# Kernel optimization log

Hardware: AMD Instinct MI355X
Metric: run time of the kernel (lower is better)

Reference implementation:

```python
import jax, jax.numpy as jnp
import numpy as np

N = 8192

def _gcn_layer(x, src, dst, W, b, norm_out, norm_in, activation=None):
    # DGL GraphConv, norm='both': D_in^{-1/2} A D_out^{-1/2} X W + b
    xw = x @ W                              # [N, out] (weight first: in>=out)
    m = (xw * norm_out[:, None])[src]       # gather per-edge messages [E, out]
    agg = jax.ops.segment_sum(m, dst, num_segments=N)
    h = agg * norm_in[:, None] + b
    return activation(h) if activation is not None else h


def setup_inputs() -> dict:
    key = jax.random.key(0)
    k1, k2, k3, k4, k5 = jax.random.split(key, 5)
    E = 262144
    in_dim, h1, h2 = 512, 256, 64
    features = jax.random.normal(k1, (N, in_dim), dtype=jnp.float32)
    src = jax.random.randint(k2, (E,), 0, N)
    dst = jax.random.randint(k3, (E,), 0, N)
    W1 = jax.random.normal(k4, (in_dim, h1), dtype=jnp.float32) / np.sqrt(in_dim)
    b1 = jnp.zeros((h1,), dtype=jnp.float32)
    W2 = jax.random.normal(k5, (h1, h2), dtype=jnp.float32) / np.sqrt(h1)
    b2 = jnp.zeros((h2,), dtype=jnp.float32)
    return {"features": features, "src": src, "dst": dst,
            "W1": W1, "b1": b1, "W2": W2, "b2": b2}


def reference(features, src, dst, W1, b1, W2, b2):
    # Degrees and symmetric normalization (clamp(min=1) as in DGL GraphConv).
    ones = jnp.ones(src.shape[0], dtype=features.dtype)
    deg_out = jax.ops.segment_sum(ones, src, num_segments=N)
    deg_in = jax.ops.segment_sum(ones, dst, num_segments=N)
    norm_out = jnp.maximum(deg_out, 1.0) ** -0.5
    norm_in = jnp.maximum(deg_in, 1.0) ** -0.5
    # Encoder (dropout is identity in eval mode).
    h = _gcn_layer(features, src, dst, W1, b1, norm_out, norm_in, jax.nn.relu)
    z = _gcn_layer(h, src, dst, W2, b2, norm_out, norm_in, None)
    # Dot-product decoder.
    adj_rec = jax.nn.sigmoid(z @ z.T)       # [N, N]
    return adj_rec
```

## Files before the change

### kernel.cpp

```cpp
#include <hip/hip_runtime.h>
#include <hip/hip_bf16.h>
#include <math.h>

#define NNODES 8192
#define NEDGES 262144
#define INDIM  512
#define H1     256
#define H2     64

typedef __attribute__((ext_vector_type(8))) short bf16x8;
typedef __attribute__((ext_vector_type(4))) float f32x4;

static __device__ __forceinline__ float bf2f(unsigned short u) {
    return __uint_as_float((unsigned)u << 16);
}
static __device__ __forceinline__ unsigned short f2bf(float f) {
    __hip_bfloat16 h = __float2bfloat16(f);
    return *(unsigned short*)&h;
}


__global__ void deg_kernel(const int* __restrict__ src, const int* __restrict__ dst,
                           int* deg_out, int* deg_in) {
    int e = blockIdx.x * blockDim.x + threadIdx.x;
    if (e < NEDGES) {
        atomicAdd(&deg_out[src[e]], 1);
        atomicAdd(&deg_in[dst[e]], 1);
    }
}

__global__ __launch_bounds__(1024) void scannorm_kernel(const int* __restrict__ deg_in,
                                                        const int* __restrict__ deg_out,
                                                        int* __restrict__ row_start,
                                                        float* __restrict__ norm_out,
                                                        float* __restrict__ norm_in) {
    __shared__ int part[1024];
    int t = threadIdx.x;
    int v[8]; int s = 0;
#pragma unroll
    for (int u = 0; u < 8; u++) { v[u] = deg_in[t * 8 + u]; s += v[u]; }
    part[t] = s; __syncthreads();
    for (int off = 1; off < 1024; off <<= 1) {
        int x = part[t];
        if (t >= off) x += part[t - off];
        __syncthreads();
        part[t] = x;
        __syncthreads();
    }
    int run = part[t] - s;
#pragma unroll
    for (int u = 0; u < 8; u++) {
        int n = t * 8 + u;
        row_start[n] = run; run += v[u];
        norm_in[n]  = 1.0f / sqrtf(fmaxf((float)v[u], 1.0f));
        norm_out[n] = 1.0f / sqrtf(fmaxf((float)deg_out[n], 1.0f));
    }
    if (t == 1023) row_start[NNODES] = run;
}

__global__ void bucket_kernel(const int* __restrict__ src, const int* __restrict__ dst,
                              const int* __restrict__ row_start,
                              int* cursor, int* __restrict__ sorted_src) {
    int e = blockIdx.x * blockDim.x + threadIdx.x;
    if (e < NEDGES) {
        int d = dst[e];
        int p = atomicAdd(&cursor[d], 1);
        sorted_src[row_start[d] + p] = src[e];
    }
}


__global__ void prep_kernel(const float* __restrict__ features, __hip_bfloat16* __restrict__ featb,
                            const float* __restrict__ W1, __hip_bfloat16* __restrict__ w1t,
                            const float* __restrict__ W2, __hip_bfloat16* __restrict__ w2t) {
    int b = blockIdx.x;
    if (b < 4096) {
        int t = b * 256 + threadIdx.x;
        float4 v = ((const float4*)features)[t];
        ushort4 o;
        o.x = f2bf(v.x); o.y = f2bf(v.y); o.z = f2bf(v.z); o.w = f2bf(v.w);
        ((ushort4*)featb)[t] = o;
    } else if (b < 4608) {
        int t = (b - 4096) * 256 + threadIdx.x;
        int k = t / H1, c = t % H1;
        w1t[(size_t)c * INDIM + k] = __float2bfloat16(W1[t]);
    } else {
        int t = (b - 4608) * 256 + threadIdx.x;
        int k = t / H2, c = t % H2;
        w2t[(size_t)c * H1 + k] = __float2bfloat16(W2[t]);
    }
}


template<int K, int MT, int NT, int NOUT>
__global__ __launch_bounds__(256) void gemm_mfma_kernel(const __hip_bfloat16* __restrict__ Af,
                                                        const __hip_bfloat16* __restrict__ BTf,
                                                        const float* __restrict__ scale,
                                                        __hip_bfloat16* __restrict__ outf) {
    constexpr int AM = MT / 64;
    constexpr int BN = NT / 16;
    const short* A  = (const short*)Af;
    const short* BT = (const short*)BTf;
    short* out = (short*)outf;
    const int lane = threadIdx.x & 63;
    const int wid  = threadIdx.x >> 6;
    const int i0 = blockIdx.y * MT + wid * (MT / 4);
    const int j0 = blockIdx.x * NT;
    const int fr = lane & 15;
    const int kg = lane >> 4;

    f32x4 acc[AM][BN] = {};
    for (int k0 = 0; k0 < K; k0 += 32) {
        bf16x8 a[AM], b[BN];
#pragma unroll
        for (int m = 0; m < AM; m++)
            a[m] = *(const bf16x8*)&A[(size_t)(i0 + m * 16 + fr) * K + k0 + kg * 8];
#pragma unroll
        for (int n = 0; n < BN; n++)
            b[n] = *(const bf16x8*)&BT[(size_t)(j0 + n * 16 + fr) * K + k0 + kg * 8];
#pragma unroll
        for (int m = 0; m < AM; m++)
#pragma unroll
            for (int n = 0; n < BN; n++)
                acc[m][n] = __builtin_amdgcn_mfma_f32_16x16x32_bf16(a[m], b[n], acc[m][n], 0, 0, 0);
    }

    const int col = lane & 15;
    const int rg4 = (lane >> 4) * 4;
#pragma unroll
    for (int m = 0; m < AM; m++)
#pragma unroll
        for (int r = 0; r < 4; r++) {
            int row = i0 + m * 16 + rg4 + r;
            float sc = scale[row];
#pragma unroll
            for (int n = 0; n < BN; n++)
                out[(size_t)row * NOUT + j0 + n * 16 + col] = f2bf(acc[m][n][r] * sc);
        }
}


__global__ void agg256_kernel(const int* __restrict__ row_start, const int* __restrict__ sorted_src,
                              const __hip_bfloat16* __restrict__ msgb, const float* __restrict__ norm_in,
                              const float* __restrict__ bias, __hip_bfloat16* __restrict__ outb) {
    const ushort4* msg = (const ushort4*)msgb;
    int n = blockIdx.x;
    int lane = threadIdx.x;
    int e0 = row_start[n], e1 = row_start[n + 1];
    float ax = 0.f, ay = 0.f, az = 0.f, aw = 0.f;
    int e = e0;
    for (; e + 1 < e1; e += 2) {
        int s0 = sorted_src[e], s1 = sorted_src[e + 1];
        ushort4 v0 = msg[(size_t)s0 * 64 + lane];
        ushort4 v1 = msg[(size_t)s1 * 64 + lane];
        ax += bf2f(v0.x) + bf2f(v1.x);
        ay += bf2f(v0.y) + bf2f(v1.y);
        az += bf2f(v0.z) + bf2f(v1.z);
        aw += bf2f(v0.w) + bf2f(v1.w);
    }
    if (e < e1) {
        ushort4 v0 = msg[(size_t)sorted_src[e] * 64 + lane];
        ax += bf2f(v0.x); ay += bf2f(v0.y); az += bf2f(v0.z); aw += bf2f(v0.w);
    }
    float ni = norm_in[n];
    float4 bb = ((const float4*)bias)[lane];
    ushort4 o;
    o.x = f2bf(fmaxf(ax * ni + bb.x, 0.f));
    o.y = f2bf(fmaxf(ay * ni + bb.y, 0.f));
    o.z = f2bf(fmaxf(az * ni + bb.z, 0.f));
    o.w = f2bf(fmaxf(aw * ni + bb.w, 0.f));
    ((ushort4*)outb)[(size_t)n * 64 + lane] = o;
}

__global__ void agg64_kernel(const int* __restrict__ row_start, const int* __restrict__ sorted_src,
                             const __hip_bfloat16* __restrict__ msgb, const float* __restrict__ norm_in,
                             const float* __restrict__ bias, __hip_bfloat16* __restrict__ outb) {
    const unsigned* msg = (const unsigned*)msgb;
    int n = blockIdx.x;
    int lane = threadIdx.x;
    int half = lane >> 5, li = lane & 31;
    int e0 = row_start[n], e1 = row_start[n + 1];
    float ax = 0.f, ay = 0.f;
    for (int e = e0 + half; e < e1; e += 2) {
        unsigned u = msg[(size_t)sorted_src[e] * 32 + li];
        ax += bf2f((unsigned short)(u & 0xffff));
        ay += bf2f((unsigned short)(u >> 16));
    }
    ax += __shfl_xor(ax, 32);
    ay += __shfl_xor(ay, 32);
    if (half == 0) {
        float ni = norm_in[n];
        float z0 = ax * ni + bias[2 * li];
        float z1 = ay * ni + bias[2 * li + 1];
        unsigned o = (unsigned)f2bf(z0) | ((unsigned)f2bf(z1) << 16);
        ((unsigned*)outb)[(size_t)n * 32 + li] = o;
    }
}


#define LSTR 132

__global__ __launch_bounds__(256) void decoder_mfma_kernel(const __hip_bfloat16* __restrict__ zbf,
                                                           float* __restrict__ out) {
    __shared__ float lds[4][16 * LSTR];
    const short* zb = (const short*)zbf;
    const int lane = threadIdx.x & 63;
    const int wid  = threadIdx.x >> 6;
    const int i0 = blockIdx.y * 128 + wid * 32;
    const int j0 = blockIdx.x * 128;
    const int fr = lane & 15;
    const int kg = lane >> 4;

    f32x4 acc[2][8] = {};
#pragma unroll
    for (int ks = 0; ks < 2; ks++) {
        bf16x8 a[2], b[8];
#pragma unroll
        for (int m = 0; m < 2; m++)
            a[m] = *(const bf16x8*)&zb[(size_t)(i0 + m * 16 + fr) * H2 + ks * 32 + kg * 8];
#pragma unroll
        for (int n = 0; n < 8; n++)
            b[n] = *(const bf16x8*)&zb[(size_t)(j0 + n * 16 + fr) * H2 + ks * 32 + kg * 8];
#pragma unroll
        for (int m = 0; m < 2; m++)
#pragma unroll
            for (int n = 0; n < 8; n++)
                acc[m][n] = __builtin_amdgcn_mfma_f32_16x16x32_bf16(a[m], b[n], acc[m][n], 0, 0, 0);
    }

    float mx = 0.f;
#pragma unroll
    for (int m = 0; m < 2; m++)
#pragma unroll
        for (int n = 0; n < 8; n++)
#pragma unroll
            for (int r = 0; r < 4; r++)
                mx = fmaxf(mx, fabsf(acc[m][n][r]));
    const bool useExp = __any(mx > 1.0f);

    const int col = lane & 15;
    const int rg4 = (lane >> 4) * 4;
    float* L = lds[wid];
    const int rrow = (lane >> 5);
    const int rcol = (lane & 31) * 4;

#pragma unroll
    for (int m = 0; m < 2; m++) {
#pragma unroll
        for (int n = 0; n < 8; n++)
#pragma unroll
            for (int r = 0; r < 4; r++) {
                float x = acc[m][n][r];
                float s;
                if (useExp) {
                    s = 1.f / (1.f + __expf(-x));
                } else {
                    float u = x * x;
                    s = 0.5f + x * (0.25f + u * (-0.0208333333f + u * 0.0020833333f));
                }
                L[(rg4 + r) * LSTR + n * 16 + col] = s;
            }
#pragma unroll
        for (int i = 0; i < 8; i++) {
            int row = i * 2 + rrow;
            float4 v = *(float4*)&L[row * LSTR + rcol];
            *(float4*)&out[(size_t)(i0 + m * 16 + row) * NNODES + j0 + rcol] = v;
        }
    }
}


extern "C" void kernel_launch(void* const* d_in, const int* in_sizes, int n_in,
                              void* d_out, int out_size, void* d_ws, size_t ws_size,
                              hipStream_t stream) {
    const float* features = (const float*)d_in[0];
    const int*   src      = (const int*)d_in[1];
    const int*   dst      = (const int*)d_in[2];
    const float* W1       = (const float*)d_in[3];
    const float* b1       = (const float*)d_in[4];
    const float* W2       = (const float*)d_in[5];
    const float* b2       = (const float*)d_in[6];
    float* out = (float*)d_out;

    char* p = (char*)d_ws;
    auto alloc = [&](size_t bytes) -> void* {
        void* q = (void*)p;
        p += (bytes + 255) & ~(size_t)255;
        return q;
    };
    int*   deg_out_i  = (int*)alloc(NNODES * 4);
    int*   deg_in_i   = (int*)alloc(NNODES * 4);
    int*   cursor     = (int*)alloc(NNODES * 4);
    int*   row_start  = (int*)alloc((NNODES + 1) * 4);
    float* norm_out   = (float*)alloc(NNODES * 4);
    float* norm_in    = (float*)alloc(NNODES * 4);
    int*   sorted_src = (int*)alloc(NEDGES * 4);
    __hip_bfloat16* featb = (__hip_bfloat16*)alloc((size_t)NNODES * INDIM * 2);
    __hip_bfloat16* w1t   = (__hip_bfloat16*)alloc((size_t)H1 * INDIM * 2);
    __hip_bfloat16* w2t   = (__hip_bfloat16*)alloc((size_t)H2 * H1 * 2);
    __hip_bfloat16* xwb   = (__hip_bfloat16*)alloc((size_t)NNODES * H1 * 2);
    __hip_bfloat16* hb    = (__hip_bfloat16*)alloc((size_t)NNODES * H1 * 2);
    __hip_bfloat16* hwb   = (__hip_bfloat16*)alloc((size_t)NNODES * H2 * 2);
    __hip_bfloat16* zb    = (__hip_bfloat16*)alloc((size_t)NNODES * H2 * 2);

    hipMemsetAsync(deg_out_i, 0, 3 * NNODES * 4, stream);

    deg_kernel<<<NEDGES / 256, 256, 0, stream>>>(src, dst, deg_out_i, deg_in_i);
    scannorm_kernel<<<1, 1024, 0, stream>>>(deg_in_i, deg_out_i, row_start, norm_out, norm_in);
    bucket_kernel<<<NEDGES / 256, 256, 0, stream>>>(src, dst, row_start, cursor, sorted_src);
    prep_kernel<<<4672, 256, 0, stream>>>(features, featb, W1, w1t, W2, w2t);

    gemm_mfma_kernel<INDIM, 128, 128, H1><<<dim3(H1 / 128, NNODES / 128), 256, 0, stream>>>(
        featb, w1t, norm_out, xwb);
    agg256_kernel<<<NNODES, 64, 0, stream>>>(row_start, sorted_src, xwb, norm_in, b1, hb);

    gemm_mfma_kernel<H1, 64, 64, H2><<<dim3(1, NNODES / 64), 256, 0, stream>>>(
        hb, w2t, norm_out, hwb);
    agg64_kernel<<<NNODES, 64, 0, stream>>>(row_start, sorted_src, hwb, norm_in, b2, zb);

    decoder_mfma_kernel<<<dim3(NNODES / 128, NNODES / 128), 256, 0, stream>>>(zb, out);
}
```

Before: 170.8 us.

## Fuse layer-1 aggregation with layer-2 projection, fold memset into prep

The layer-1 aggregation kernel now keeps each node's 256-wide hidden row in shared memory and multiplies it by W2 with scalar FMAs, writing the 64-wide projected row directly. This removes the intermediate h buffer round trip and the separate second GEMM launch. The degree memset is folded into the prep kernel as extra blocks, and the first GEMM tile is shrunk from 128x128 to 64x64 for more blocks. The fused matvec runs on scalar ALUs rather than MFMA and re-reads W2 for every node, which could cost more than the launch and traffic it saves.

```diff
diff --git a/kernel.cpp b/kernel.cpp
--- a/kernel.cpp
+++ b/kernel.cpp
@@ -20,59 +20,10 @@
 }
 
 
-__global__ void deg_kernel(const int* __restrict__ src, const int* __restrict__ dst,
-                           int* deg_out, int* deg_in) {
-    int e = blockIdx.x * blockDim.x + threadIdx.x;
-    if (e < NEDGES) {
-        atomicAdd(&deg_out[src[e]], 1);
-        atomicAdd(&deg_in[dst[e]], 1);
-    }
-}
-
-__global__ __launch_bounds__(1024) void scannorm_kernel(const int* __restrict__ deg_in,
-                                                        const int* __restrict__ deg_out,
-                                                        int* __restrict__ row_start,
-                                                        float* __restrict__ norm_out,
-                                                        float* __restrict__ norm_in) {
-    __shared__ int part[1024];
-    int t = threadIdx.x;
-    int v[8]; int s = 0;
-#pragma unroll
-    for (int u = 0; u < 8; u++) { v[u] = deg_in[t * 8 + u]; s += v[u]; }
-    part[t] = s; __syncthreads();
-    for (int off = 1; off < 1024; off <<= 1) {
-        int x = part[t];
-        if (t >= off) x += part[t - off];
-        __syncthreads();
-        part[t] = x;
-        __syncthreads();
-    }
-    int run = part[t] - s;
-#pragma unroll
-    for (int u = 0; u < 8; u++) {
-        int n = t * 8 + u;
-        row_start[n] = run; run += v[u];
-        norm_in[n]  = 1.0f / sqrtf(fmaxf((float)v[u], 1.0f));
-        norm_out[n] = 1.0f / sqrtf(fmaxf((float)deg_out[n], 1.0f));
-    }
-    if (t == 1023) row_start[NNODES] = run;
-}
-
-__global__ void bucket_kernel(const int* __restrict__ src, const int* __restrict__ dst,
-                              const int* __restrict__ row_start,
-                              int* cursor, int* __restrict__ sorted_src) {
-    int e = blockIdx.x * blockDim.x + threadIdx.x;
-    if (e < NEDGES) {
-        int d = dst[e];
-        int p = atomicAdd(&cursor[d], 1);
-        sorted_src[row_start[d] + p] = src[e];
-    }
-}
-
-
 __global__ void prep_kernel(const float* __restrict__ features, __hip_bfloat16* __restrict__ featb,
                             const float* __restrict__ W1, __hip_bfloat16* __restrict__ w1t,
-                            const float* __restrict__ W2, __hip_bfloat16* __restrict__ w2t) {
+                            const float* __restrict__ W2, __hip_bfloat16* __restrict__ w2t,
+                            int* __restrict__ zero_base) {
     int b = blockIdx.x;
     if (b < 4096) {
         int t = b * 256 + threadIdx.x;
@@ -84,10 +35,63 @@
         int t = (b - 4096) * 256 + threadIdx.x;
         int k = t / H1, c = t % H1;
         w1t[(size_t)c * INDIM + k] = __float2bfloat16(W1[t]);
-    } else {
+    } else if (b < 4672) {
         int t = (b - 4608) * 256 + threadIdx.x;
         int k = t / H2, c = t % H2;
         w2t[(size_t)c * H1 + k] = __float2bfloat16(W2[t]);
+    } else {
+        int t = (b - 4672) * 256 + threadIdx.x;
+        ((int4*)zero_base)[t] = make_int4(0, 0, 0, 0);
+    }
+}
+
+
+__global__ void deg_kernel(const int* __restrict__ src, const int* __restrict__ dst,
+                           int* deg_out, int* deg_in) {
+    int e = blockIdx.x * blockDim.x + threadIdx.x;
+    if (e < NEDGES) {
+        atomicAdd(&deg_out[src[e]], 1);
+        atomicAdd(&deg_in[dst[e]], 1);
+    }
+}
+
+__global__ __launch_bounds__(1024) void scannorm_kernel(const int* __restrict__ deg_in,
+                                                        const int* __restrict__ deg_out,
+                                                        int* __restrict__ row_start,
+                                                        float* __restrict__ norm_out,
+                                                        float* __restrict__ norm_in) {
+    __shared__ int part[1024];
+    int t = threadIdx.x;
+    int v[8]; int s = 0;
+#pragma unroll
+    for (int u = 0; u < 8; u++) { v[u] = deg_in[t * 8 + u]; s += v[u]; }
+    part[t] = s; __syncthreads();
+    for (int off = 1; off < 1024; off <<= 1) {
+        int x = part[t];
+        if (t >= off) x += part[t - off];
+        __syncthreads();
+        part[t] = x;
+        __syncthreads();
+    }
+    int run = part[t] - s;
+#pragma unroll
+    for (int u = 0; u < 8; u++) {
+        int n = t * 8 + u;
+        row_start[n] = run; run += v[u];
+        norm_in[n]  = 1.0f / sqrtf(fmaxf((float)v[u], 1.0f));
+        norm_out[n] = 1.0f / sqrtf(fmaxf((float)deg_out[n], 1.0f));
+    }
+    if (t == 1023) row_start[NNODES] = run;
+}
+
+__global__ void bucket_kernel(const int* __restrict__ src, const int* __restrict__ dst,
+                              const int* __restrict__ row_start,
+                              int* cursor, int* __restrict__ sorted_src) {
+    int e = blockIdx.x * blockDim.x + threadIdx.x;
+    if (e < NEDGES) {
+        int d = dst[e];
+        int p = atomicAdd(&cursor[d], 1);
+        sorted_src[row_start[d] + p] = src[e];
     }
 }
 
@@ -140,9 +144,12 @@
 }
 
 
-__global__ void agg256_kernel(const int* __restrict__ row_start, const int* __restrict__ sorted_src,
-                              const __hip_bfloat16* __restrict__ msgb, const float* __restrict__ norm_in,
-                              const float* __restrict__ bias, __hip_bfloat16* __restrict__ outb) {
+__global__ void aggfused_kernel(const int* __restrict__ row_start, const int* __restrict__ sorted_src,
+                                const __hip_bfloat16* __restrict__ msgb,
+                                const float* __restrict__ norm_in, const float* __restrict__ norm_out,
+                                const float* __restrict__ b1, const __hip_bfloat16* __restrict__ w2t,
+                                __hip_bfloat16* __restrict__ hwb) {
+    __shared__ float hs[H1];
     const ushort4* msg = (const ushort4*)msgb;
     int n = blockIdx.x;
     int lane = threadIdx.x;
@@ -163,14 +170,30 @@
         ax += bf2f(v0.x); ay += bf2f(v0.y); az += bf2f(v0.z); aw += bf2f(v0.w);
     }
     float ni = norm_in[n];
-    float4 bb = ((const float4*)bias)[lane];
-    ushort4 o;
-    o.x = f2bf(fmaxf(ax * ni + bb.x, 0.f));
-    o.y = f2bf(fmaxf(ay * ni + bb.y, 0.f));
-    o.z = f2bf(fmaxf(az * ni + bb.z, 0.f));
-    o.w = f2bf(fmaxf(aw * ni + bb.w, 0.f));
-    ((ushort4*)outb)[(size_t)n * 64 + lane] = o;
-}
+    float4 bb = ((const float4*)b1)[lane];
+    float4 h;
+    h.x = fmaxf(ax * ni + bb.x, 0.f);
+    h.y = fmaxf(ay * ni + bb.y, 0.f);
+    h.z = fmaxf(az * ni + bb.z, 0.f);
+    h.w = fmaxf(aw * ni + bb.w, 0.f);
+    *(float4*)&hs[lane * 4] = h;
+    __syncthreads();
+
+    const short* wrow = (const short*)&w2t[(size_t)lane * H1];
+    float acc = 0.f;
+#pragma unroll
+    for (int k8 = 0; k8 < H1 / 8; k8++) {
+        bf16x8 w8 = *(const bf16x8*)&wrow[k8 * 8];
+        float4 h0 = *(const float4*)&hs[k8 * 8];
+        float4 h1 = *(const float4*)&hs[k8 * 8 + 4];
+        acc += h0.x * bf2f((unsigned short)w8[0]) + h0.y * bf2f((unsigned short)w8[1])
+             + h0.z * bf2f((unsigned short)w8[2]) + h0.w * bf2f((unsigned short)w8[3])
+             + h1.x * bf2f((unsigned short)w8[4]) + h1.y * bf2f((unsigned short)w8[5])
+             + h1.z * bf2f((unsigned short)w8[6]) + h1.w * bf2f((unsigned short)w8[7]);
+    }
+    hwb[(size_t)n * H2 + lane] = __float2bfloat16(acc * norm_out[n]);
+}
+
 
 __global__ void agg64_kernel(const int* __restrict__ row_start, const int* __restrict__ sorted_src,
                              const __hip_bfloat16* __restrict__ msgb, const float* __restrict__ norm_in,
@@ -299,23 +322,18 @@
     __hip_bfloat16* w1t   = (__hip_bfloat16*)alloc((size_t)H1 * INDIM * 2);
     __hip_bfloat16* w2t   = (__hip_bfloat16*)alloc((size_t)H2 * H1 * 2);
     __hip_bfloat16* xwb   = (__hip_bfloat16*)alloc((size_t)NNODES * H1 * 2);
-    __hip_bfloat16* hb    = (__hip_bfloat16*)alloc((size_t)NNODES * H1 * 2);
     __hip_bfloat16* hwb   = (__hip_bfloat16*)alloc((size_t)NNODES * H2 * 2);
     __hip_bfloat16* zb    = (__hip_bfloat16*)alloc((size_t)NNODES * H2 * 2);
 
-    hipMemsetAsync(deg_out_i, 0, 3 * NNODES * 4, stream);
-
+    prep_kernel<<<4696, 256, 0, stream>>>(features, featb, W1, w1t, W2, w2t, deg_out_i);
     deg_kernel<<<NEDGES / 256, 256, 0, stream>>>(src, dst, deg_out_i, deg_in_i);
     scannorm_kernel<<<1, 1024, 0, stream>>>(deg_in_i, deg_out_i, row_start, norm_out, norm_in);
     bucket_kernel<<<NEDGES / 256, 256, 0, stream>>>(src, dst, row_start, cursor, sorted_src);
-    prep_kernel<<<4672, 256, 0, stream>>>(features, featb, W1, w1t, W2, w2t);
-
-    gemm_mfma_kernel<INDIM, 128, 128, H1><<<dim3(H1 / 128, NNODES / 128), 256, 0, stream>>>(
+
+    gemm_mfma_kernel<INDIM, 64, 64, H1><<<dim3(H1 / 64, NNODES / 64), 256, 0, stream>>>(
         featb, w1t, norm_out, xwb);
-    agg256_kernel<<<NNODES, 64, 0, stream>>>(row_start, sorted_src, xwb, norm_in, b1, hb);
-
-    gemm_mfma_kernel<H1, 64, 64, H2><<<dim3(1, NNODES / 64), 256, 0, stream>>>(
-        hb, w2t, norm_out, hwb);
+    aggfused_kernel<<<NNODES, 64, 0, stream>>>(row_start, sorted_src, xwb, norm_in, norm_out,
+                                               b1, w2t, hwb);
     agg64_kernel<<<NNODES, 64, 0, stream>>>(row_start, sorted_src, hwb, norm_in, b2, zb);
 
     decoder_mfma_kernel<<<dim3(NNODES / 128, NNODES / 128), 256, 0, stream>>>(zb, out);
```

After: 184.4 us. +7.9%, slower.

## Merge degree count into prep, bucketing with GEMM1, and agg256 with GEMM2

Applied to the files above, without the earlier changes.

Folds the degree-count atomics into the conversion/prep kernel and runs edge bucketing alongside the first GEMM as extra blocks of one launch. It also fuses the layer-1 aggregation with the second GEMM through shared memory, so the intermediate h matrix is never written to global memory. This cuts launch count and global traffic. The trade-offs are a smaller 64x64 tile for GEMM1, which loses some reuse, and a 1024-thread aggregation block whose GEMM phase uses only 4 of its 16 waves.

```diff
diff --git a/kernel.cpp b/kernel.cpp
--- a/kernel.cpp
+++ b/kernel.cpp
@@ -20,59 +20,11 @@
 }
 
 
-__global__ void deg_kernel(const int* __restrict__ src, const int* __restrict__ dst,
-                           int* deg_out, int* deg_in) {
-    int e = blockIdx.x * blockDim.x + threadIdx.x;
-    if (e < NEDGES) {
-        atomicAdd(&deg_out[src[e]], 1);
-        atomicAdd(&deg_in[dst[e]], 1);
-    }
-}
-
-__global__ __launch_bounds__(1024) void scannorm_kernel(const int* __restrict__ deg_in,
-                                                        const int* __restrict__ deg_out,
-                                                        int* __restrict__ row_start,
-                                                        float* __restrict__ norm_out,
-                                                        float* __restrict__ norm_in) {
-    __shared__ int part[1024];
-    int t = threadIdx.x;
-    int v[8]; int s = 0;
-#pragma unroll
-    for (int u = 0; u < 8; u++) { v[u] = deg_in[t * 8 + u]; s += v[u]; }
-    part[t] = s; __syncthreads();
-    for (int off = 1; off < 1024; off <<= 1) {
-        int x = part[t];
-        if (t >= off) x += part[t - off];
-        __syncthreads();
-        part[t] = x;
-        __syncthreads();
-    }
-    int run = part[t] - s;
-#pragma unroll
-    for (int u = 0; u < 8; u++) {
-        int n = t * 8 + u;
-        row_start[n] = run; run += v[u];
-        norm_in[n]  = 1.0f / sqrtf(fmaxf((float)v[u], 1.0f));
-        norm_out[n] = 1.0f / sqrtf(fmaxf((float)deg_out[n], 1.0f));
-    }
-    if (t == 1023) row_start[NNODES] = run;
-}
-
-__global__ void bucket_kernel(const int* __restrict__ src, const int* __restrict__ dst,
-                              const int* __restrict__ row_start,
-                              int* cursor, int* __restrict__ sorted_src) {
-    int e = blockIdx.x * blockDim.x + threadIdx.x;
-    if (e < NEDGES) {
-        int d = dst[e];
-        int p = atomicAdd(&cursor[d], 1);
-        sorted_src[row_start[d] + p] = src[e];
-    }
-}
-
-
-__global__ void prep_kernel(const float* __restrict__ features, __hip_bfloat16* __restrict__ featb,
-                            const float* __restrict__ W1, __hip_bfloat16* __restrict__ w1t,
-                            const float* __restrict__ W2, __hip_bfloat16* __restrict__ w2t) {
+__global__ void prepdeg_kernel(const float* __restrict__ features, __hip_bfloat16* __restrict__ featb,
+                               const float* __restrict__ W1, __hip_bfloat16* __restrict__ w1t,
+                               const float* __restrict__ W2, __hip_bfloat16* __restrict__ w2t,
+                               const int* __restrict__ src, const int* __restrict__ dst,
+                               int* deg_out, int* deg_in) {
     int b = blockIdx.x;
     if (b < 4096) {
         int t = b * 256 + threadIdx.x;
@@ -84,28 +36,58 @@
         int t = (b - 4096) * 256 + threadIdx.x;
         int k = t / H1, c = t % H1;
         w1t[(size_t)c * INDIM + k] = __float2bfloat16(W1[t]);
-    } else {
+    } else if (b < 4672) {
         int t = (b - 4608) * 256 + threadIdx.x;
         int k = t / H2, c = t % H2;
         w2t[(size_t)c * H1 + k] = __float2bfloat16(W2[t]);
-    }
+    } else {
+        int e = (b - 4672) * 256 + threadIdx.x;
+        atomicAdd(&deg_out[src[e]], 1);
+        atomicAdd(&deg_in[dst[e]], 1);
+    }
+}
+
+
+__global__ __launch_bounds__(1024) void scannorm_kernel(const int* __restrict__ deg_in,
+                                                        const int* __restrict__ deg_out,
+                                                        int* __restrict__ row_start,
+                                                        float* __restrict__ norm_out,
+                                                        float* __restrict__ norm_in) {
+    __shared__ int part[1024];
+    int t = threadIdx.x;
+    int v[8]; int s = 0;
+#pragma unroll
+    for (int u = 0; u < 8; u++) { v[u] = deg_in[t * 8 + u]; s += v[u]; }
+    part[t] = s; __syncthreads();
+    for (int off = 1; off < 1024; off <<= 1) {
+        int x = part[t];
+        if (t >= off) x += part[t - off];
+        __syncthreads();
+        part[t] = x;
+        __syncthreads();
+    }
+    int run = part[t] - s;
+#pragma unroll
+    for (int u = 0; u < 8; u++) {
+        int n = t * 8 + u;
+        row_start[n] = run; run += v[u];
+        norm_in[n]  = 1.0f / sqrtf(fmaxf((float)v[u], 1.0f));
+        norm_out[n] = 1.0f / sqrtf(fmaxf((float)deg_out[n], 1.0f));
+    }
+    if (t == 1023) row_start[NNODES] = run;
 }
 
 
 template<int K, int MT, int NT, int NOUT>
-__global__ __launch_bounds__(256) void gemm_mfma_kernel(const __hip_bfloat16* __restrict__ Af,
-                                                        const __hip_bfloat16* __restrict__ BTf,
-                                                        const float* __restrict__ scale,
-                                                        __hip_bfloat16* __restrict__ outf) {
+__device__ __forceinline__ void gemm_tile(const short* __restrict__ A, const short* __restrict__ BT,
+                                          const float* __restrict__ scale, short* __restrict__ out,
+                                          int bx, int by, int tid) {
     constexpr int AM = MT / 64;
     constexpr int BN = NT / 16;
-    const short* A  = (const short*)Af;
-    const short* BT = (const short*)BTf;
-    short* out = (short*)outf;
-    const int lane = threadIdx.x & 63;
-    const int wid  = threadIdx.x >> 6;
-    const int i0 = blockIdx.y * MT + wid * (MT / 4);
-    const int j0 = blockIdx.x * NT;
+    const int lane = tid & 63;
+    const int wid  = tid >> 6;
+    const int i0 = by * MT + wid * (MT / 4);
+    const int j0 = bx * NT;
     const int fr = lane & 15;
     const int kg = lane >> 4;
 
@@ -140,37 +122,90 @@
 }
 
 
-__global__ void agg256_kernel(const int* __restrict__ row_start, const int* __restrict__ sorted_src,
-                              const __hip_bfloat16* __restrict__ msgb, const float* __restrict__ norm_in,
-                              const float* __restrict__ bias, __hip_bfloat16* __restrict__ outb) {
+__global__ __launch_bounds__(256) void bucketgemm_kernel(const int* __restrict__ src, const int* __restrict__ dst,
+                                                         const int* __restrict__ row_start, int* cursor,
+                                                         int* __restrict__ sorted_src,
+                                                         const __hip_bfloat16* __restrict__ featb,
+                                                         const __hip_bfloat16* __restrict__ w1t,
+                                                         const float* __restrict__ norm_out,
+                                                         __hip_bfloat16* __restrict__ xwb) {
+    int b = blockIdx.x;
+    if (b < 1024) {
+        int e = b * 256 + threadIdx.x;
+        int d = dst[e];
+        int p = atomicAdd(&cursor[d], 1);
+        sorted_src[row_start[d] + p] = src[e];
+    } else {
+        int g = b - 1024;
+        gemm_tile<INDIM, 64, 64, H1>((const short*)featb, (const short*)w1t, norm_out,
+                                     (short*)xwb, g & 3, g >> 2, threadIdx.x);
+    }
+}
+
+
+__global__ __launch_bounds__(1024) void agg_gemm2_kernel(const int* __restrict__ row_start,
+                                                         const int* __restrict__ sorted_src,
+                                                         const __hip_bfloat16* __restrict__ msgb,
+                                                         const float* __restrict__ norm_in,
+                                                         const float* __restrict__ norm_out,
+                                                         const float* __restrict__ b1,
+                                                         const __hip_bfloat16* __restrict__ w2t,
+                                                         __hip_bfloat16* __restrict__ hwb) {
+    __shared__ short hs[16][H1 + 8];
     const ushort4* msg = (const ushort4*)msgb;
-    int n = blockIdx.x;
-    int lane = threadIdx.x;
-    int e0 = row_start[n], e1 = row_start[n + 1];
-    float ax = 0.f, ay = 0.f, az = 0.f, aw = 0.f;
-    int e = e0;
-    for (; e + 1 < e1; e += 2) {
-        int s0 = sorted_src[e], s1 = sorted_src[e + 1];
-        ushort4 v0 = msg[(size_t)s0 * 64 + lane];
-        ushort4 v1 = msg[(size_t)s1 * 64 + lane];
-        ax += bf2f(v0.x) + bf2f(v1.x);
-        ay += bf2f(v0.y) + bf2f(v1.y);
-        az += bf2f(v0.z) + bf2f(v1.z);
-        aw += bf2f(v0.w) + bf2f(v1.w);
-    }
-    if (e < e1) {
-        ushort4 v0 = msg[(size_t)sorted_src[e] * 64 + lane];
-        ax += bf2f(v0.x); ay += bf2f(v0.y); az += bf2f(v0.z); aw += bf2f(v0.w);
-    }
-    float ni = norm_in[n];
-    float4 bb = ((const float4*)bias)[lane];
-    ushort4 o;
-    o.x = f2bf(fmaxf(ax * ni + bb.x, 0.f));
-    o.y = f2bf(fmaxf(ay * ni + bb.y, 0.f));
-    o.z = f2bf(fmaxf(az * ni + bb.z, 0.f));
-    o.w = f2bf(fmaxf(aw * ni + bb.w, 0.f));
-    ((ushort4*)outb)[(size_t)n * 64 + lane] = o;
-}
+    const int wid  = threadIdx.x >> 6;
+    const int lane = threadIdx.x & 63;
+    const int n0 = blockIdx.x * 16;
+    {
+        int n = n0 + wid;
+        int e0 = row_start[n], e1 = row_start[n + 1];
+        float ax = 0.f, ay = 0.f, az = 0.f, aw = 0.f;
+        int e = e0;
+        for (; e + 1 < e1; e += 2) {
+            int s0 = sorted_src[e], s1 = sorted_src[e + 1];
+            ushort4 v0 = msg[(size_t)s0 * 64 + lane];
+            ushort4 v1 = msg[(size_t)s1 * 64 + lane];
+            ax += bf2f(v0.x) + bf2f(v1.x);
+            ay += bf2f(v0.y) + bf2f(v1.y);
+            az += bf2f(v0.z) + bf2f(v1.z);
+            aw += bf2f(v0.w) + bf2f(v1.w);
+        }
+        if (e < e1) {
+            ushort4 v0 = msg[(size_t)sorted_src[e] * 64 + lane];
+            ax += bf2f(v0.x); ay += bf2f(v0.y); az += bf2f(v0.z); aw += bf2f(v0.w);
+        }
+        float ni = norm_in[n];
+        float4 bb = ((const float4*)b1)[lane];
+        ushort4 o;
+        o.x = f2bf(fmaxf(ax * ni + bb.x, 0.f));
+        o.y = f2bf(fmaxf(ay * ni + bb.y, 0.f));
+        o.z = f2bf(fmaxf(az * ni + bb.z, 0.f));
+        o.w = f2bf(fmaxf(aw * ni + bb.w, 0.f));
+        *(ushort4*)&hs[wid][lane * 4] = o;
+    }
+    __syncthreads();
+    if (wid < 4) {
+        const short* BT = (const short*)w2t;
+        const int fr = lane & 15;
+        const int kg = lane >> 4;
+        const int j0 = wid * 16;
+        f32x4 acc = {};
+#pragma unroll
+        for (int k0 = 0; k0 < H1; k0 += 32) {
+            bf16x8 a = *(const bf16x8*)&hs[fr][k0 + kg * 8];
+            bf16x8 b = *(const bf16x8*)&BT[(size_t)(j0 + fr) * H1 + k0 + kg * 8];
+            acc = __builtin_amdgcn_mfma_f32_16x16x32_bf16(a, b, acc, 0, 0, 0);
+        }
+        const int col = lane & 15;
+        const int rg4 = (lane >> 4) * 4;
+#pragma unroll
+        for (int r = 0; r < 4; r++) {
+            int nn = n0 + rg4 + r;
+            hwb[(size_t)nn * H2 + j0 + col] = __float2bfloat16(acc[r] * norm_out[nn]);
+        }
+    }
+}
+
 
 __global__ void agg64_kernel(const int* __restrict__ row_start, const int* __restrict__ sorted_src,
                              const __hip_bfloat16* __restrict__ msgb, const float* __restrict__ norm_in,
@@ -299,24 +334,20 @@
     __hip_bfloat16* w1t   = (__hip_bfloat16*)alloc((size_t)H1 * INDIM * 2);
     __hip_bfloat16* w2t   = (__hip_bfloat16*)alloc((size_t)H2 * H1 * 2);
     __hip_bfloat16* xwb   = (__hip_bfloat16*)alloc((size_t)NNODES * H1 * 2);
-    __hip_bfloat16* hb    = (__hip_bfloat16*)alloc((size_t)NNODES * H1 * 2);
     __hip_bfloat16* hwb   = (__hip_bfloat16*)alloc((size_t)NNODES * H2 * 2);
     __hip_bfloat16* zb    = (__hip_bfloat16*)alloc((size_t)NNODES * H2 * 2);
 
     hipMemsetAsync(deg_out_i, 0, 3 * NNODES * 4, stream);
-
-    deg_kernel<<<NEDGES / 256, 256, 0, stream>>>(src, dst, deg_out_i, deg_in_i);
-    scannorm_kernel<<<1, 1024, 0, stream>>>(deg_in_i, deg_out_i, row_start, norm_out, norm_in);
-    bucket_kernel<<<NEDGES / 256, 256, 0, stream>>>(src, dst, row_start, cursor, sorted_src);
-    prep_kernel<<<4672, 256, 0, stream>>>(features, featb, W1, w1t, W2, w2t);
-
-    gemm_mfma_kernel<INDIM, 128, 128, H1><<<dim3(H1 / 128, NNODES / 128), 256, 0, stream>>>(
-        featb, w1t, norm_out, xwb);
-    agg256_kernel<<<NNODES, 64, 0, stream>>>(row_start, sorted_src, xwb, norm_in, b1, hb);
-
-    gemm_mfma_kernel<H1, 64, 64, H2><<<dim3(1, NNODES / 64), 256, 0, stream>>>(
-        hb, w2t, norm_out, hwb);
-    agg64_kernel<<<NNODES, 64, 0, stream>>>(row_start, sorted_src, hwb, norm_in, b2, zb);
-
-    decoder_mfma_kernel<<<dim3(NNODES / 128, NNODES / 128), 256, 0, stream>>>(zb, out);
-}
+    prepdeg_kernel<<<4672 + NEDGES / 256, 256, 0, stream>>>(
+        features, featb, W1, w1t, W2, w2t, src, dst, deg_out_i, deg_in_i);
+    scannorm_kernel<<<1, 1024, 0, stream>>>(deg_in_i, deg_out_i,
+                                            row_start, norm_out, norm_in);
+    bucketgemm_kernel<<<1024 + 512, 256, 0, stream>>>(
+        src, dst, row_start, cursor, sorted_src, featb, w1t, norm_out, xwb);
+    agg_gemm2_kernel<<<NNODES / 16, 1024, 0, stream>>>(
+        row_start, sorted_src, xwb, norm_in, norm_out, b1, w2t, hwb);
+    agg64_kernel<<<NNODES, 64, 0, stream>>>(row_start, sorted_src, hwb,
+                                            norm_in, b2, zb);
+    decoder_mfma_kernel<<<dim3(NNODES / 128, NNODES / 128), 256, 0, stream>>>(
+        zb, out);
+}
```

Measured after the change: 181.3 us. +6.1%, slower.

## Fuse graph preprocessing, GCN layers and decoder into one cooperative persistent kernel

Applied to the files above, without the earlier changes.

Replaces the chain of separate launches (degree count, scan, bucketing, two GEMMs, two aggregations, decoder) with one cooperative kernel of 512 blocks that uses grid-wide syncs between phases. The first GEMM now overlaps with edge bucketing, and the decoder runs persistently with 8 tiles per block. This removes per-launch overhead and idle gaps between dependent small kernels. In exchange, each phase is limited to 512 blocks, GEMM1 tiles shrink to 64x64, and every grid.sync adds a barrier cost. If the cooperative launch fails, the old multi-kernel path runs instead.

```diff
diff --git a/kernel.cpp b/kernel.cpp
--- a/kernel.cpp
+++ b/kernel.cpp
@@ -1,12 +1,16 @@
 #include <hip/hip_runtime.h>
+#include <hip/hip_cooperative_groups.h>
 #include <hip/hip_bf16.h>
 #include <math.h>
+
+namespace cg = cooperative_groups;
 
 #define NNODES 8192
 #define NEDGES 262144
 #define INDIM  512
 #define H1     256
 #define H2     64
+#define LSTR   132
 
 typedef __attribute__((ext_vector_type(8))) short bf16x8;
 typedef __attribute__((ext_vector_type(4))) float f32x4;
@@ -17,56 +21,6 @@
 static __device__ __forceinline__ unsigned short f2bf(float f) {
     __hip_bfloat16 h = __float2bfloat16(f);
     return *(unsigned short*)&h;
-}
-
-
-__global__ void deg_kernel(const int* __restrict__ src, const int* __restrict__ dst,
-                           int* deg_out, int* deg_in) {
-    int e = blockIdx.x * blockDim.x + threadIdx.x;
-    if (e < NEDGES) {
-        atomicAdd(&deg_out[src[e]], 1);
-        atomicAdd(&deg_in[dst[e]], 1);
-    }
-}
-
-__global__ __launch_bounds__(1024) void scannorm_kernel(const int* __restrict__ deg_in,
-                                                        const int* __restrict__ deg_out,
-                                                        int* __restrict__ row_start,
-                                                        float* __restrict__ norm_out,
-                                                        float* __restrict__ norm_in) {
-    __shared__ int part[1024];
-    int t = threadIdx.x;
-    int v[8]; int s = 0;
-#pragma unroll
-    for (int u = 0; u < 8; u++) { v[u] = deg_in[t * 8 + u]; s += v[u]; }
-    part[t] = s; __syncthreads();
-    for (int off = 1; off < 1024; off <<= 1) {
-        int x = part[t];
-        if (t >= off) x += part[t - off];
-        __syncthreads();
-        part[t] = x;
-        __syncthreads();
-    }
-    int run = part[t] - s;
-#pragma unroll
-    for (int u = 0; u < 8; u++) {
-        int n = t * 8 + u;
-        row_start[n] = run; run += v[u];
-        norm_in[n]  = 1.0f / sqrtf(fmaxf((float)v[u], 1.0f));
-        norm_out[n] = 1.0f / sqrtf(fmaxf((float)deg_out[n], 1.0f));
-    }
-    if (t == 1023) row_start[NNODES] = run;
-}
-
-__global__ void bucket_kernel(const int* __restrict__ src, const int* __restrict__ dst,
-                              const int* __restrict__ row_start,
-                              int* cursor, int* __restrict__ sorted_src) {
-    int e = blockIdx.x * blockDim.x + threadIdx.x;
-    if (e < NEDGES) {
-        int d = dst[e];
-        int p = atomicAdd(&cursor[d], 1);
-        sorted_src[row_start[d] + p] = src[e];
-    }
 }
 
 
@@ -93,52 +47,308 @@
 
 
 template<int K, int MT, int NT, int NOUT>
+__device__ __forceinline__ void gemm_tile(const short* __restrict__ A, const short* __restrict__ BT,
+                                          const float* __restrict__ scale, short* __restrict__ out,
+                                          int bx, int by, int tid) {
+    constexpr int AM = MT / 64;
+    constexpr int BN = NT / 16;
+    const int lane = tid & 63;
+    const int wid  = tid >> 6;
+    const int i0 = by * MT + wid * (MT / 4);
+    const int j0 = bx * NT;
+    const int fr = lane & 15;
+    const int kg = lane >> 4;
+
+    f32x4 acc[AM][BN] = {};
+    for (int k0 = 0; k0 < K; k0 += 32) {
+        bf16x8 a[AM], b[BN];
+#pragma unroll
+        for (int m = 0; m < AM; m++)
+            a[m] = *(const bf16x8*)&A[(size_t)(i0 + m * 16 + fr) * K + k0 + kg * 8];
+#pragma unroll
+        for (int n = 0; n < BN; n++)
+            b[n] = *(const bf16x8*)&BT[(size_t)(j0 + n * 16 + fr) * K + k0 + kg * 8];
+#pragma unroll
+        for (int m = 0; m < AM; m++)
+#pragma unroll
+            for (int n = 0; n < BN; n++)
+                acc[m][n] = __builtin_amdgcn_mfma_f32_16x16x32_bf16(a[m], b[n], acc[m][n], 0, 0, 0);
+    }
+
+    const int col = lane & 15;
+    const int rg4 = (lane >> 4) * 4;
+#pragma unroll
+    for (int m = 0; m < AM; m++)
+#pragma unroll
+        for (int r = 0; r < 4; r++) {
+            int row = i0 + m * 16 + rg4 + r;
+            float sc = scale[row];
+#pragma unroll
+            for (int n = 0; n < BN; n++)
+                out[(size_t)row * NOUT + j0 + n * 16 + col] = f2bf(acc[m][n][r] * sc);
+        }
+}
+
+
+__global__ __launch_bounds__(256, 2) void mega_kernel(
+    const int* __restrict__ src, const int* __restrict__ dst,
+    int* deg_out, int* deg_in, int* cursor,
+    int* __restrict__ row_start, float* __restrict__ norm_out, float* __restrict__ norm_in,
+    int* __restrict__ sorted_src,
+    const __hip_bfloat16* __restrict__ featb, const __hip_bfloat16* __restrict__ w1t,
+    const __hip_bfloat16* __restrict__ w2t,
+    const float* __restrict__ b1, const float* __restrict__ b2,
+    __hip_bfloat16* __restrict__ xwb, __hip_bfloat16* __restrict__ hb,
+    __hip_bfloat16* __restrict__ hwb, __hip_bfloat16* __restrict__ zb,
+    float* __restrict__ out) {
+
+    cg::grid_group grid = cg::this_grid();
+    __shared__ float ldsbuf[4][16 * LSTR];
+    const int tid  = threadIdx.x;
+    const int gtid = blockIdx.x * 256 + tid;
+    const int lane = tid & 63;
+    const int widx = tid >> 6;
+
+    if (gtid < 3 * NNODES) deg_out[gtid] = 0;
+    grid.sync();
+
+    {
+        int e = gtid;
+        atomicAdd(&deg_out[src[e]], 1);
+        atomicAdd(&deg_in[dst[e]], 1);
+        e = gtid + 131072;
+        atomicAdd(&deg_out[src[e]], 1);
+        atomicAdd(&deg_in[dst[e]], 1);
+    }
+    grid.sync();
+
+    if (blockIdx.x == 0) {
+        int* part = (int*)ldsbuf;
+        int s = 0;
+        for (int u = 0; u < 32; u++) s += deg_in[tid * 32 + u];
+        part[tid] = s; __syncthreads();
+        for (int off = 1; off < 256; off <<= 1) {
+            int x = part[tid];
+            if (tid >= off) x += part[tid - off];
+            __syncthreads();
+            part[tid] = x;
+            __syncthreads();
+        }
+        int run = part[tid] - s;
+        for (int u = 0; u < 32; u++) {
+            int n = tid * 32 + u;
+            int d = deg_in[n];
+            row_start[n] = run; run += d;
+            norm_in[n]  = 1.0f / sqrtf(fmaxf((float)d, 1.0f));
+            norm_out[n] = 1.0f / sqrtf(fmaxf((float)deg_out[n], 1.0f));
+        }
+        if (tid == 255) row_start[NNODES] = run;
+    }
+    grid.sync();
+
+    {
+        int e = gtid;
+        int d = dst[e];
+        int p = atomicAdd(&cursor[d], 1);
+        sorted_src[row_start[d] + p] = src[e];
+        e = gtid + 131072;
+        d = dst[e];
+        p = atomicAdd(&cursor[d], 1);
+        sorted_src[row_start[d] + p] = src[e];
+    }
+    gemm_tile<INDIM, 64, 64, H1>((const short*)featb, (const short*)w1t, norm_out,
+                                 (short*)xwb, blockIdx.x & 3, blockIdx.x >> 2, tid);
+    grid.sync();
+
+    {
+        const ushort4* msg = (const ushort4*)xwb;
+        int wave = (blockIdx.x << 2) | widx;
+        for (int n = wave; n < NNODES; n += 2048) {
+            int e0 = row_start[n], e1 = row_start[n + 1];
+            float ax = 0.f, ay = 0.f, az = 0.f, aw = 0.f;
+            int e = e0;
+            for (; e + 1 < e1; e += 2) {
+                int s0 = sorted_src[e], s1 = sorted_src[e + 1];
+                ushort4 v0 = msg[(size_t)s0 * 64 + lane];
+                ushort4 v1 = msg[(size_t)s1 * 64 + lane];
+                ax += bf2f(v0.x) + bf2f(v1.x);
+                ay += bf2f(v0.y) + bf2f(v1.y);
+                az += bf2f(v0.z) + bf2f(v1.z);
+                aw += bf2f(v0.w) + bf2f(v1.w);
+            }
+            if (e < e1) {
+                ushort4 v0 = msg[(size_t)sorted_src[e] * 64 + lane];
+                ax += bf2f(v0.x); ay += bf2f(v0.y); az += bf2f(v0.z); aw += bf2f(v0.w);
+            }
+            float ni = norm_in[n];
+            float4 bb = ((const float4*)b1)[lane];
+            ushort4 o;
+            o.x = f2bf(fmaxf(ax * ni + bb.x, 0.f));
+            o.y = f2bf(fmaxf(ay * ni + bb.y, 0.f));
+            o.z = f2bf(fmaxf(az * ni + bb.z, 0.f));
+            o.w = f2bf(fmaxf(aw * ni + bb.w, 0.f));
+            ((ushort4*)hb)[(size_t)n * 64 + lane] = o;
+        }
+    }
+    grid.sync();
+
+    if (blockIdx.x < 128)
+        gemm_tile<H1, 64, 64, H2>((const short*)hb, (const short*)w2t, norm_out,
+                                  (short*)hwb, 0, blockIdx.x, tid);
+    grid.sync();
+
+    {
+        const unsigned* msg = (const unsigned*)hwb;
+        int wave = (blockIdx.x << 2) | widx;
+        int half = lane >> 5, li = lane & 31;
+        for (int n = wave; n < NNODES; n += 2048) {
+            int e0 = row_start[n], e1 = row_start[n + 1];
+            float ax = 0.f, ay = 0.f;
+            for (int e = e0 + half; e < e1; e += 2) {
+                unsigned u = msg[(size_t)sorted_src[e] * 32 + li];
+                ax += bf2f((unsigned short)(u & 0xffff));
+                ay += bf2f((unsigned short)(u >> 16));
+            }
+            ax += __shfl_xor(ax, 32);
+            ay += __shfl_xor(ay, 32);
+            if (half == 0) {
+                float ni = norm_in[n];
+                float z0 = ax * ni + b2[2 * li];
+                float z1 = ay * ni + b2[2 * li + 1];
+                unsigned o = (unsigned)f2bf(z0) | ((unsigned)f2bf(z1) << 16);
+                ((unsigned*)zb)[(size_t)n * 32 + li] = o;
+            }
+        }
+    }
+    grid.sync();
+
+    {
+        const short* z = (const short*)zb;
+        const int fr = lane & 15;
+        const int kg = lane >> 4;
+        const int col = lane & 15;
+        const int rg4 = (lane >> 4) * 4;
+        float* L = ldsbuf[widx];
+        const int rrow = lane >> 5;
+        const int rcol = (lane & 31) * 4;
+
+        for (int s = 0; s < 8; s++) {
+            int t = blockIdx.x * 8 + s;
+            const int i0 = (t >> 6) * 128 + widx * 32;
+            const int j0 = (t & 63) * 128;
+
+            f32x4 acc[2][8] = {};
+#pragma unroll
+            for (int ks = 0; ks < 2; ks++) {
+                bf16x8 a[2], b[8];
+#pragma unroll
+                for (int m = 0; m < 2; m++)
+                    a[m] = *(const bf16x8*)&z[(size_t)(i0 + m * 16 + fr) * H2 + ks * 32 + kg * 8];
+#pragma unroll
+                for (int n = 0; n < 8; n++)
+                    b[n] = *(const bf16x8*)&z[(size_t)(j0 + n * 16 + fr) * H2 + ks * 32 + kg * 8];
+#pragma unroll
+                for (int m = 0; m < 2; m++)
+#pragma unroll
+                    for (int n = 0; n < 8; n++)
+                        acc[m][n] = __builtin_amdgcn_mfma_f32_16x16x32_bf16(a[m], b[n], acc[m][n], 0, 0, 0);
+            }
+
+            float mx = 0.f;
+#pragma unroll
+            for (int m = 0; m < 2; m++)
+#pragma unroll
+                for (int n = 0; n < 8; n++)
+#pragma unroll
+                    for (int r = 0; r < 4; r++)
+                        mx = fmaxf(mx, fabsf(acc[m][n][r]));
+            const bool useExp = __any(mx > 1.0f);
+
+#pragma unroll
+            for (int m = 0; m < 2; m++) {
+#pragma unroll
+                for (int n = 0; n < 8; n++)
+#pragma unroll
+                    for (int r = 0; r < 4; r++) {
+                        float x = acc[m][n][r];
+                        float sg;
+                        if (useExp) {
+                            sg = 1.f / (1.f + __expf(-x));
+                        } else {
+                            float u = x * x;
+                            sg = 0.5f + x * (0.25f + u * (-0.0208333333f + u * 0.0020833333f));
+                        }
+                        L[(rg4 + r) * LSTR + n * 16 + col] = sg;
+                    }
+#pragma unroll
+                for (int i = 0; i < 8; i++) {
+                    int row = i * 2 + rrow;
+                    float4 v = *(float4*)&L[row * LSTR + rcol];
+                    *(float4*)&out[(size_t)(i0 + m * 16 + row) * NNODES + j0 + rcol] = v;
+                }
+            }
+        }
+    }
+}
+
+
+__global__ void deg_kernel(const int* __restrict__ src, const int* __restrict__ dst,
+                           int* deg_out, int* deg_in) {
+    int e = blockIdx.x * blockDim.x + threadIdx.x;
+    if (e < NEDGES) {
+        atomicAdd(&deg_out[src[e]], 1);
+        atomicAdd(&deg_in[dst[e]], 1);
+    }
+}
+
+__global__ __launch_bounds__(1024) void scannorm_kernel(const int* __restrict__ deg_in,
+                                                        const int* __restrict__ deg_out,
+                                                        int* __restrict__ row_start,
+                                                        float* __restrict__ norm_out,
+                                                        float* __restrict__ norm_in) {
+    __shared__ int part[1024];
+    int t = threadIdx.x;
+    int v[8]; int s = 0;
+#pragma unroll
+    for (int u = 0; u < 8; u++) { v[u] = deg_in[t * 8 + u]; s += v[u]; }
+    part[t] = s; __syncthreads();
+    for (int off = 1; off < 1024; off <<= 1) {
+        int x = part[t];
+        if (t >= off) x += part[t - off];
+        __syncthreads();
+        part[t] = x;
+        __syncthreads();
+    }
+    int run = part[t] - s;
+#pragma unroll
+    for (int u = 0; u < 8; u++) {
+        int n = t * 8 + u;
+        row_start[n] = run; run += v[u];
+        norm_in[n]  = 1.0f / sqrtf(fmaxf((float)v[u], 1.0f));
+        norm_out[n] = 1.0f / sqrtf(fmaxf((float)deg_out[n], 1.0f));
+    }
+    if (t == 1023) row_start[NNODES] = run;
+}
+
+__global__ void bucket_kernel(const int* __restrict__ src, const int* __restrict__ dst,
+                              const int* __restrict__ row_start,
+                              int* cursor, int* __restrict__ sorted_src) {
+    int e = blockIdx.x * blockDim.x + threadIdx.x;
+    if (e < NEDGES) {
+        int d = dst[e];
+        int p = atomicAdd(&cursor[d], 1);
+        sorted_src[row_start[d] + p] = src[e];
+    }
+}
+
+template<int K, int MT, int NT, int NOUT>
 __global__ __launch_bounds__(256) void gemm_mfma_kernel(const __hip_bfloat16* __restrict__ Af,
                                                         const __hip_bfloat16* __restrict__ BTf,
                                                         const float* __restrict__ scale,
                                                         __hip_bfloat16* __restrict__ outf) {
-    constexpr int AM = MT / 64;
-    constexpr int BN = NT / 16;
-    const short* A  = (const short*)Af;
-    const short* BT = (const short*)BTf;
-    short* out = (short*)outf;
-    const int lane = threadIdx.x & 63;
-    const int wid  = threadIdx.x >> 6;
-    const int i0 = blockIdx.y * MT + wid * (MT / 4);
-    const int j0 = blockIdx.x * NT;
-    const int fr = lane & 15;
-    const int kg = lane >> 4;
-
-    f32x4 acc[AM][BN] = {};
-    for (int k0 = 0; k0 < K; k0 += 32) {
-        bf16x8 a[AM], b[BN];
-#pragma unroll
-        for (int m = 0; m < AM; m++)
-            a[m] = *(const bf16x8*)&A[(size_t)(i0 + m * 16 + fr) * K + k0 + kg * 8];
-#pragma unroll
-        for (int n = 0; n < BN; n++)
-            b[n] = *(const bf16x8*)&BT[(size_t)(j0 + n * 16 + fr) * K + k0 + kg * 8];
-#pragma unroll
-        for (int m = 0; m < AM; m++)
-#pragma unroll
-            for (int n = 0; n < BN; n++)
-                acc[m][n] = __builtin_amdgcn_mfma_f32_16x16x32_bf16(a[m], b[n], acc[m][n], 0, 0, 0);
-    }
-
-    const int col = lane & 15;
-    const int rg4 = (lane >> 4) * 4;
-#pragma unroll
-    for (int m = 0; m < AM; m++)
-#pragma unroll
-        for (int r = 0; r < 4; r++) {
-            int row = i0 + m * 16 + rg4 + r;
-            float sc = scale[row];
-#pragma unroll
-            for (int n = 0; n < BN; n++)
-                out[(size_t)row * NOUT + j0 + n * 16 + col] = f2bf(acc[m][n][r] * sc);
-        }
-}
-
+    gemm_tile<K, MT, NT, NOUT>((const short*)Af, (const short*)BTf, scale, (short*)outf,
+                               blockIdx.x, blockIdx.y, threadIdx.x);
+}
 
 __global__ void agg256_kernel(const int* __restrict__ row_start, const int* __restrict__ sorted_src,
                               const __hip_bfloat16* __restrict__ msgb, const float* __restrict__ norm_in,
@@ -197,9 +407,6 @@
     }
 }
 
-
-#define LSTR 132
-
 __global__ __launch_bounds__(256) void decoder_mfma_kernel(const __hip_bfloat16* __restrict__ zbf,
                                                            float* __restrict__ out) {
     __shared__ float lds[4][16 * LSTR];
@@ -241,7 +448,7 @@
     const int col = lane & 15;
     const int rg4 = (lane >> 4) * 4;
     float* L = lds[wid];
-    const int rrow = (lane >> 5);
+    const int rrow = lane >> 5;
     const int rcol = (lane & 31) * 4;
 
 #pragma unroll
@@ -303,20 +510,27 @@
     __hip_bfloat16* hwb   = (__hip_bfloat16*)alloc((size_t)NNODES * H2 * 2);
     __hip_bfloat16* zb    = (__hip_bfloat16*)alloc((size_t)NNODES * H2 * 2);
 
-    hipMemsetAsync(deg_out_i, 0, 3 * NNODES * 4, stream);
-
-    deg_kernel<<<NEDGES / 256, 256, 0, stream>>>(src, dst, deg_out_i, deg_in_i);
-    scannorm_kernel<<<1, 1024, 0, stream>>>(deg_in_i, deg_out_i, row_start, norm_out, norm_in);
-    bucket_kernel<<<NEDGES / 256, 256, 0, stream>>>(src, dst, row_start, cursor, sorted_src);
     prep_kernel<<<4672, 256, 0, stream>>>(features, featb, W1, w1t, W2, w2t);
 
-    gemm_mfma_kernel<INDIM, 128, 128, H1><<<dim3(H1 / 128, NNODES / 128), 256, 0, stream>>>(
-        featb, w1t, norm_out, xwb);
-    agg256_kernel<<<NNODES, 64, 0, stream>>>(row_start, sorted_src, xwb, norm_in, b1, hb);
-
-    gemm_mfma_kernel<H1, 64, 64, H2><<<dim3(1, NNODES / 64), 256, 0, stream>>>(
-        hb, w2t, norm_out, hwb);
-    agg64_kernel<<<NNODES, 64, 0, stream>>>(row_start, sorted_src, hwb, norm_in, b2, zb);
-
-    decoder_mfma_kernel<<<dim3(NNODES / 128, NNODES / 128), 256, 0, stream>>>(zb, out);
-}
+    void* args[] = {
+        (void*)&src, (void*)&dst, (void*)&deg_out_i, (void*)&deg_in_i, (void*)&cursor,
+        (void*)&row_start, (void*)&norm_out, (void*)&norm_in, (void*)&sorted_src,
+        (void*)&featb, (void*)&w1t, (void*)&w2t, (void*)&b1, (void*)&b2,
+        (void*)&xwb, (void*)&hb, (void*)&hwb, (void*)&zb, (void*)&out
+    };
+    hipError_t err = hipLaunchCooperativeKernel((const void*)mega_kernel,
+                                                dim3(512), dim3(256), args, 0, stream);
+    if (err != hipSuccess) {
+        hipMemsetAsync(deg_out_i, 0, 3 * NNODES * 4, stream);
+        deg_kernel<<<NEDGES / 256, 256, 0, stream>>>(src, dst, deg_out_i, deg_in_i);
+        scannorm_kernel<<<1, 1024, 0, stream>>>(deg_in_i, deg_out_i, row_start, norm_out, norm_in);
+        bucket_kernel<<<NEDGES / 256, 256, 0, stream>>>(src, dst, row_start, cursor, sorted_src);
+        gemm_mfma_kernel<INDIM, 64, 64, H1><<<dim3(H1 / 64, NNODES / 64), 256, 0, stream>>>(
+            featb, w1t, norm_out, xwb);
+        agg256_kernel<<<NNODES, 64, 0, stream>>>(row_start, sorted_src, xwb, norm_in, b1, hb);
+        gemm_mfma_kernel<H1, 64, 64, H2><<<dim3(1, NNODES / 64), 256, 0, stream>>>(
+            hb, w2t, norm_out, hwb);
+        agg64_kernel<<<NNODES, 64, 0, stream>>>(row_start, sorted_src, hwb, norm_in, b2, zb);
+        decoder_mfma_kernel<<<dim3(NNODES / 128, NNODES / 128), 256, 0, stream>>>(zb, out);
+    }
+}
```

Measured after the change: 618.8 us. +262.2%, slower.
